# Performance work log

Hardware: AMD Instinct MI355X
Metric: run time of the kernel (lower is better)

The kernel has to match this reference:

```python
import jax, jax.numpy as jnp
import numpy as np

EPS = 1e-5

def inorm(x):
    # InstanceNorm1d(0) on 2D input: per-row normalization over last dim, biased var, no affine
    m = jnp.mean(x, axis=1, keepdims=True)
    v = jnp.mean((x - m) ** 2, axis=1, keepdims=True)
    return (x - m) / jnp.sqrt(v + EPS)

def spmm(rows, cols, vals, x, n_rows):
    # COO sparse @ dense: gather source rows, scale by edge weight, scatter-add to dest rows
    return jax.ops.segment_sum(vals[:, None] * x[cols], rows, num_segments=n_rows)

def setup_inputs() -> dict:
    key = jax.random.key(0)
    ks = jax.random.split(key, 16)
    NG, NI, D, E = 50000, 100000, 128, 800000
    B = 65536
    s = 0.1
    return {
        "group_ids": jax.random.randint(ks[0], (B,), 0, NG),
        "item_ids": jax.random.randint(ks[1], (B,), 0, NI),
        "gi_rows": jnp.sort(jax.random.randint(ks[2], (E,), 0, NG)),
        "gi_cols": jax.random.randint(ks[3], (E,), 0, NI),
        "gi_vals": jax.random.uniform(ks[4], (E,)),
        "gg_rows": jnp.sort(jax.random.randint(ks[5], (E,), 0, NG)),
        "gg_cols": jax.random.randint(ks[6], (E,), 0, NG),
        "gg_vals": jax.random.uniform(ks[7], (E,)),
        "g_feat": jax.random.normal(ks[8], (NG, D)),
        "i_feat": jax.random.normal(ks[9], (NI, D)),
        "emb_group": s * jax.random.normal(ks[10], (NG, D)),
        "emb_item": s * jax.random.normal(ks[11], (NI, D)),
        "W_w": s * jax.random.normal(ks[12], (D, D)),
        "W_b": jnp.zeros((D,)),
        "red_w": s * jax.random.normal(ks[13], (D, D)),
        "red_b": jnp.zeros((D,)),
        "item_fus_w": s * jax.random.normal(ks[14], (D, 2 * D)),
        "item_fus_b": jnp.zeros((D,)),
        "group_fus_w": s * jax.random.normal(ks[15], (D, 2 * D)),
        "group_fus_b": jnp.zeros((D,)),
    }

def reference(group_ids, item_ids, gi_rows, gi_cols, gi_vals, gg_rows, gg_cols, gg_vals,
              g_feat, i_feat, emb_group, emb_item, W_w, W_b, red_w, red_b,
              item_fus_w, item_fus_b, group_fus_w, group_fus_b):
    NG = g_feat.shape[0]
    L = 2
    sig = jax.nn.sigmoid

    def social_layer(x):
        # relu(W(spmm(gg, x)))
        agg = spmm(gg_rows, gg_cols, gg_vals, x, NG)
        return jax.nn.relu(agg @ W_w.T + W_b)

    # constructTrainGraph
    g2 = inorm(inorm(g_feat) @ red_w.T + red_b)
    i2 = inorm(inorm(i_feat) @ red_w.T + red_b)
    final_item = sig(jnp.concatenate([emb_item, i2], axis=1) @ item_fus_w.T + item_fus_b)
    g_from_items = sig(spmm(gi_rows, gi_cols, gi_vals, final_item, NG))
    fus_group = sig(jnp.concatenate([emb_group, g2], axis=1) @ group_fus_w.T + group_fus_b)
    first = sig(social_layer(fus_group))
    tmp = g_from_items + first
    second = sig(social_layer(first))
    tmp = tmp + second
    final_group = sig(tmp / L)

    # forward scoring
    all_neighbors = spmm(gg_rows, gg_cols, gg_vals, final_group, NG)
    ge = final_group[group_ids]
    ie = final_item[item_ids]
    ne = all_neighbors[group_ids]
    gamma = jnp.sum(ge * ie, axis=1)
    gamma_2 = jnp.sum(ne * ge, axis=1) + jnp.sum(ne * ie, axis=1)
    return gamma, gamma_2
```

## Files before the change

kernel.cpp:

```cpp
#include <hip/hip_runtime.h>
#include <hip/hip_bf16.h>

typedef __hip_bfloat16 bf16;
typedef __attribute__((ext_vector_type(8))) short bf16x8;
typedef __attribute__((ext_vector_type(4))) float f32x4;

#define D128 128

__device__ __forceinline__ float sigf(float x) {
    float e = __builtin_amdgcn_exp2f(-1.44269504f * x);
    return __builtin_amdgcn_rcpf(1.0f + e);
}

__device__ __forceinline__ short bf2s(bf16 h) { union { bf16 h; short s; } u; u.h = h; return u.s; }
__device__ __forceinline__ float s2f(short s) { union { short s; bf16 h; } u; u.s = s; return __bfloat162float(u.h); }

__device__ __forceinline__ float loadf(const void* p, size_t off, int isbf) {
    return isbf ? __bfloat162float(((const bf16*)p)[off]) : ((const float*)p)[off];
}

__global__ __launch_bounds__(256) void sniff_kernel(const unsigned short* __restrict__ g,
                                                    int* __restrict__ cnt) {
    int t = threadIdx.x;
    int c = 0;
    for (int i = t; i < 16384; i += 256) {
        unsigned short u = g[i];
        if ((u & 0x7F80u) == 0x7F80u) c++;
    }
    #pragma unroll
    for (int o = 32; o >= 1; o >>= 1) c += __shfl_xor(c, o);
    __shared__ int sh[4];
    if ((t & 63) == 0) sh[t >> 6] = c;
    __syncthreads();
    if (t == 0) *cnt = sh[0] + sh[1] + sh[2] + sh[3];
}

template <int KCH>
__global__ __launch_bounds__(256) void prep_w(const void* __restrict__ W,
                                              bf16x8* __restrict__ wf,
                                              const void* __restrict__ bias,
                                              float* __restrict__ bias_f,
                                              const int* __restrict__ cnt) {
    int isbf = (*cnt == 0);
    const int K = KCH * 32;
    int idx = blockIdx.x * 256 + threadIdx.x;
    const int total = 8 * KCH * 64;
    if (idx < total) {
        int t = idx / (KCH * 64);
        int c = (idx / 64) % KCH;
        int l = idx & 63;
        int row = t * 16 + (l & 15);
        int off = c * 32 + (l >> 4) * 8;
        bf16x8 r;
        if (isbf) {
            r = *reinterpret_cast<const bf16x8*>((const bf16*)W + (size_t)row * K + off);
        } else {
            const f32x4* f = reinterpret_cast<const f32x4*>((const float*)W + (size_t)row * K + off);
            f32x4 a = f[0], b = f[1];
            #pragma unroll
            for (int j = 0; j < 4; ++j) {
                r[j] = bf2s(__float2bfloat16(a[j]));
                r[4 + j] = bf2s(__float2bfloat16(b[j]));
            }
        }
        wf[idx] = r;
    }
    if (idx < D128) bias_f[idx] = loadf(bias, idx, isbf);
}

__global__ __launch_bounds__(256) void ngn_kernel(const void* __restrict__ X,
                                                  const bf16x8* __restrict__ wf,
                                                  const float* __restrict__ bias_f,
                                                  bf16* __restrict__ out, int N,
                                                  const int* __restrict__ cnt) {
    int isbf = (*cnt == 0);
    int tid = threadIdx.x;
    int wave = tid >> 6, lane = tid & 63;
    int quad = lane >> 4, l16 = lane & 15;
    int tile = blockIdx.x * 4 + wave;
    if (tile * 16 >= N) return;
    int mrow = tile * 16 + l16;

    float x[4][8];
    if (isbf) {
        #pragma unroll
        for (int c = 0; c < 4; ++c) {
            bf16x8 v = *reinterpret_cast<const bf16x8*>(
                (const bf16*)X + (size_t)mrow * D128 + c * 32 + quad * 8);
            #pragma unroll
            for (int j = 0; j < 8; ++j) x[c][j] = s2f(v[j]);
        }
    } else {
        #pragma unroll
        for (int c = 0; c < 4; ++c) {
            const f32x4* f = reinterpret_cast<const f32x4*>(
                (const float*)X + (size_t)mrow * D128 + c * 32 + quad * 8);
            f32x4 a = f[0], b = f[1];
            #pragma unroll
            for (int j = 0; j < 4; ++j) { x[c][j] = a[j]; x[c][4 + j] = b[j]; }
        }
    }
    float s = 0.f, ss = 0.f;
    #pragma unroll
    for (int c = 0; c < 4; ++c)
        #pragma unroll
        for (int j = 0; j < 8; ++j) { s += x[c][j]; ss += x[c][j] * x[c][j]; }
    s += __shfl_xor(s, 16); ss += __shfl_xor(ss, 16);
    s += __shfl_xor(s, 32); ss += __shfl_xor(ss, 32);
    float mean = s * (1.0f / 128.0f);
    float var = ss * (1.0f / 128.0f) - mean * mean;
    float rinv = rsqrtf(fmaxf(var, 0.f) + 1e-5f);

    bf16x8 af[4];
    #pragma unroll
    for (int c = 0; c < 4; ++c)
        #pragma unroll
        for (int j = 0; j < 8; ++j)
            af[c][j] = bf2s(__float2bfloat16((x[c][j] - mean) * rinv));

    f32x4 acc[8] = {};
    #pragma unroll
    for (int t = 0; t < 8; ++t)
        #pragma unroll
        for (int c = 0; c < 4; ++c)
            acc[t] = __builtin_amdgcn_mfma_f32_16x16x32_bf16(
                af[c], wf[(t * 4 + c) * 64 + lane], acc[t], 0, 0, 0);

    float vals[8][4];
    float ps[4] = {0, 0, 0, 0}, pss[4] = {0, 0, 0, 0};
    #pragma unroll
    for (int t = 0; t < 8; ++t) {
        float b = bias_f[t * 16 + l16];
        #pragma unroll
        for (int i = 0; i < 4; ++i) {
            float v = acc[t][i] + b;
            vals[t][i] = v;
            ps[i] += v; pss[i] += v * v;
        }
    }
    #pragma unroll
    for (int i = 0; i < 4; ++i) {
        #pragma unroll
        for (int o = 1; o < 16; o <<= 1) {
            ps[i] += __shfl_xor(ps[i], o);
            pss[i] += __shfl_xor(pss[i], o);
        }
    }
    #pragma unroll
    for (int i = 0; i < 4; ++i) {
        int row = tile * 16 + quad * 4 + i;
        float m2 = ps[i] * (1.0f / 128.0f);
        float v2 = pss[i] * (1.0f / 128.0f) - m2 * m2;
        float r2 = rsqrtf(fmaxf(v2, 0.f) + 1e-5f);
        #pragma unroll
        for (int t = 0; t < 8; ++t)
            out[(size_t)row * D128 + t * 16 + l16] =
                __float2bfloat16((vals[t][i] - m2) * r2);
    }
}

template <int KCH, int ACT, int A0T>
__global__ __launch_bounds__(256) void gemm_kernel(const void* __restrict__ A0,
                                                   const bf16* __restrict__ A1,
                                                   const bf16x8* __restrict__ wf,
                                                   const float* __restrict__ bias_f,
                                                   bf16* __restrict__ out, int N,
                                                   const int* __restrict__ cnt) {
    int isbf = (*cnt == 0);
    int tid = threadIdx.x;
    int wave = tid >> 6, lane = tid & 63;
    int quad = lane >> 4, l16 = lane & 15;
    int tile = blockIdx.x * 4 + wave;
    if (tile * 16 >= N) return;
    int mrow = tile * 16 + l16;

    bool a0bf = (A0T == 2) || (A0T == 1 && isbf);
    const int na = (KCH == 8) ? 4 : KCH;
    bf16x8 af[KCH];
    if (KCH == 8) {
        #pragma unroll
        for (int c = 4; c < KCH; ++c)
            af[c] = *reinterpret_cast<const bf16x8*>(
                A1 + (size_t)mrow * D128 + (c - 4) * 32 + quad * 8);
    }
    if (a0bf) {
        #pragma unroll
        for (int c = 0; c < na; ++c)
            af[c] = *reinterpret_cast<const bf16x8*>(
                (const bf16*)A0 + (size_t)mrow * D128 + c * 32 + quad * 8);
    } else {
        #pragma unroll
        for (int c = 0; c < na; ++c) {
            const f32x4* f = reinterpret_cast<const f32x4*>(
                (const float*)A0 + (size_t)mrow * D128 + c * 32 + quad * 8);
            f32x4 a = f[0], b = f[1];
            #pragma unroll
            for (int j = 0; j < 4; ++j) {
                af[c][j] = bf2s(__float2bfloat16(a[j]));
                af[c][4 + j] = bf2s(__float2bfloat16(b[j]));
            }
        }
    }

    f32x4 acc[8] = {};
    #pragma unroll
    for (int t = 0; t < 8; ++t)
        #pragma unroll
        for (int c = 0; c < KCH; ++c)
            acc[t] = __builtin_amdgcn_mfma_f32_16x16x32_bf16(
                af[c], wf[(t * KCH + c) * 64 + lane], acc[t], 0, 0, 0);

    #pragma unroll
    for (int t = 0; t < 8; ++t) {
        float b = bias_f[t * 16 + l16];
        #pragma unroll
        for (int i = 0; i < 4; ++i) {
            int row = tile * 16 + quad * 4 + i;
            float v = acc[t][i] + b;
            if (ACT == 1) v = sigf(v);
            else if (ACT == 2) v = sigf(fmaxf(v, 0.0f));
            out[(size_t)row * D128 + t * 16 + l16] = __float2bfloat16(v);
        }
    }
}

__global__ __launch_bounds__(256) void rowptr_kernel(const int* __restrict__ rows,
                                                     int* __restrict__ ptr,
                                                     int NR, int E) {
    int r = blockIdx.x * 256 + threadIdx.x;
    if (r > NR) return;
    int lo = 0, hi = E;
    while (lo < hi) {
        int mid = (lo + hi) >> 1;
        if (rows[mid] < r) lo = mid + 1; else hi = mid;
    }
    ptr[r] = lo;
}

#define SPMM_U 16
#define SPMM_RPW 4

template <int FM>
__device__ __forceinline__ void st_row(void* __restrict__ out, int r,
                                       int lane, float a0, float a1,
                                       const bf16* __restrict__ f1,
                                       const bf16* __restrict__ f2) {
    if (FM == 0) {
        float2 v; v.x = a0; v.y = a1;
        ((float2*)((float*)out + (size_t)r * D128))[lane] = v;
    } else if (FM == 1) {
        __hip_bfloat162 h;
        h.x = __float2bfloat16(a0);
        h.y = __float2bfloat16(a1);
        ((__hip_bfloat162*)((bf16*)out + (size_t)r * D128))[lane] = h;
    } else {
        __hip_bfloat162 h1 = ((const __hip_bfloat162*)(f1 + (size_t)r * D128))[lane];
        __hip_bfloat162 h2 = ((const __hip_bfloat162*)(f2 + (size_t)r * D128))[lane];
        float v0 = (sigf(a0) + __bfloat162float(h1.x) + __bfloat162float(h2.x)) * 0.5f;
        float v1 = (sigf(a1) + __bfloat162float(h1.y) + __bfloat162float(h2.y)) * 0.5f;
        __hip_bfloat162 h;
        h.x = __float2bfloat16(sigf(v0));
        h.y = __float2bfloat16(sigf(v1));
        ((__hip_bfloat162*)((bf16*)out + (size_t)r * D128))[lane] = h;
    }
}

template <int FM>
__device__ __forceinline__ void spmm_core(const int* __restrict__ rows,
                                          const int* __restrict__ ptr,
                                          const int* __restrict__ cols,
                                          const void* __restrict__ vals,
                                          const bf16* __restrict__ X,
                                          void* __restrict__ out,
                                          int r0, int r1, int lane, int isbf,
                                          const bf16* __restrict__ f1,
                                          const bf16* __restrict__ f2) {
    int e0 = __builtin_amdgcn_readfirstlane(ptr[r0]);
    int e1 = __builtin_amdgcn_readfirstlane(ptr[r1]);

    if (e0 == e1) {
        for (int z = r0; z < r1; ++z) st_row<FM>(out, z, lane, 0.f, 0.f, f1, f2);
        return;
    }

    int prev = __builtin_amdgcn_readfirstlane(rows[e0]);
    for (int z = r0; z < prev; ++z) st_row<FM>(out, z, lane, 0.f, 0.f, f1, f2);

    int u16 = lane & 15, grp = lane >> 4;
    int emax = e1 - 1;

    auto meta_ld = [&](int base) -> unsigned int {
        int e = base + u16;
        if (e > emax) e = emax;
        unsigned int v = 0;
        if (grp == 0) v = (unsigned int)cols[e];
        else if (grp == 1) v = (unsigned int)rows[e];
        else if (grp == 2)
            v = isbf ? (((unsigned int)((const unsigned short*)vals)[e]) << 16)
                     : ((const unsigned int*)vals)[e];
        return v;
    };

    unsigned int mv = meta_ld(e0);
    float a0 = 0.f, a1 = 0.f;
    for (int base = e0; base < e1; base += SPMM_U) {
        int nb = e1 - base;
        unsigned int xr[SPMM_U];
        #pragma unroll
        for (int u = 0; u < SPMM_U; ++u) {
            int cc = __builtin_amdgcn_readlane(mv, u);
            xr[u] = *((const unsigned int*)(X + (size_t)(unsigned)cc * D128) + lane);
        }
        int rr[SPMM_U];
        float vv[SPMM_U];
        #pragma unroll
        for (int u = 0; u < SPMM_U; ++u) {
            rr[u] = __builtin_amdgcn_readlane(mv, 16 + u);
            unsigned int vb = __builtin_amdgcn_readlane(mv, 32 + u);
            vv[u] = (u < nb) ? __uint_as_float(vb) : 0.f;
        }
        int nbase = base + SPMM_U;
        if (nbase < e1) mv = meta_ld(nbase);
        #pragma unroll
        for (int u = 0; u < SPMM_U; ++u) {
            if (rr[u] != prev) {
                st_row<FM>(out, prev, lane, a0, a1, f1, f2);
                for (int z = prev + 1; z < rr[u]; ++z)
                    st_row<FM>(out, z, lane, 0.f, 0.f, f1, f2);
                a0 = 0.f; a1 = 0.f;
                prev = rr[u];
            }
            __hip_bfloat162 x2 = *reinterpret_cast<const __hip_bfloat162*>(&xr[u]);
            a0 += vv[u] * __bfloat162float(x2.x);
            a1 += vv[u] * __bfloat162float(x2.y);
        }
    }
    st_row<FM>(out, prev, lane, a0, a1, f1, f2);
    for (int z = prev + 1; z < r1; ++z) st_row<FM>(out, z, lane, 0.f, 0.f, f1, f2);
}

template <int OUTBF>
__global__ __launch_bounds__(256) void spmm_hyb_kernel(const int* __restrict__ rows,
                                                       const int* __restrict__ ptr,
                                                       const int* __restrict__ cols,
                                                       const void* __restrict__ vals,
                                                       const bf16* __restrict__ X,
                                                       void* __restrict__ out, int NR,
                                                       const int* __restrict__ cnt) {
    int isbf = (*cnt == 0);
    int w = blockIdx.x * 4 + (threadIdx.x >> 6);
    int r0 = w * SPMM_RPW;
    if (r0 >= NR) return;
    int r1 = min(r0 + SPMM_RPW, NR);
    int lane = threadIdx.x & 63;
    spmm_core<OUTBF ? 1 : 0>(rows, ptr, cols, vals, X, out, r0, r1, lane, isbf,
                             nullptr, nullptr);
}

__global__ __launch_bounds__(256) void spmm_fg_kernel(const int* __restrict__ rows,
                                                      const int* __restrict__ ptr,
                                                      const int* __restrict__ cols,
                                                      const void* __restrict__ vals,
                                                      const bf16* __restrict__ X,
                                                      const bf16* __restrict__ f1,
                                                      const bf16* __restrict__ f2,
                                                      bf16* __restrict__ out, int NR,
                                                      const int* __restrict__ cnt) {
    int isbf = (*cnt == 0);
    int w = blockIdx.x * 4 + (threadIdx.x >> 6);
    int r0 = w * SPMM_RPW;
    if (r0 >= NR) return;
    int r1 = min(r0 + SPMM_RPW, NR);
    int lane = threadIdx.x & 63;
    spmm_core<3>(rows, ptr, cols, vals, X, out, r0, r1, lane, isbf, f1, f2);
}

__global__ __launch_bounds__(256) void score_kernel(const int* __restrict__ gids,
                                                    const int* __restrict__ iids,
                                                    const bf16* __restrict__ FG,
                                                    const bf16* __restrict__ FI,
                                                    const float* __restrict__ NB,
                                                    void* __restrict__ out, int Bn,
                                                    const int* __restrict__ cnt) {
    int isbf = (*cnt == 0);
    int w = blockIdx.x * 4 + (threadIdx.x >> 6);
    int lane = threadIdx.x & 63;
    if (w >= Bn) return;
    int g = gids[w];
    int it = iids[w];
    __hip_bfloat162 ge2 = ((const __hip_bfloat162*)(FG + (size_t)g * D128))[lane];
    __hip_bfloat162 ie2 = ((const __hip_bfloat162*)(FI + (size_t)it * D128))[lane];
    float2 ne2 = ((const float2*)(NB + (size_t)g * D128))[lane];
    float ge0 = __bfloat162float(ge2.x), ge1 = __bfloat162float(ge2.y);
    float ie0 = __bfloat162float(ie2.x), ie1 = __bfloat162float(ie2.y);
    float gi = ge0 * ie0 + ge1 * ie1;
    float ng = ne2.x * ge0 + ne2.y * ge1;
    float ni = ne2.x * ie0 + ne2.y * ie1;
    #pragma unroll
    for (int o = 32; o >= 1; o >>= 1) {
        gi += __shfl_xor(gi, o);
        ng += __shfl_xor(ng, o);
        ni += __shfl_xor(ni, o);
    }
    if (lane == 0) {
        if (isbf) {
            ((bf16*)out)[w] = __float2bfloat16(gi);
            ((bf16*)out)[Bn + w] = __float2bfloat16(ng + ni);
        } else {
            ((float*)out)[w] = gi;
            ((float*)out)[Bn + w] = ng + ni;
        }
    }
}

extern "C" void kernel_launch(void* const* d_in, const int* in_sizes, int n_in,
                              void* d_out, int out_size, void* d_ws, size_t ws_size,
                              hipStream_t stream) {
    const int* group_ids = (const int*)d_in[0];
    const int* item_ids  = (const int*)d_in[1];
    const int* gi_rows   = (const int*)d_in[2];
    const int* gi_cols   = (const int*)d_in[3];
    const void* gi_vals  = d_in[4];
    const int* gg_rows   = (const int*)d_in[5];
    const int* gg_cols   = (const int*)d_in[6];
    const void* gg_vals  = d_in[7];
    const void* g_feat   = d_in[8];
    const void* i_feat   = d_in[9];
    const void* emb_group = d_in[10];
    const void* emb_item  = d_in[11];
    const void* W_w       = d_in[12];
    const void* W_b       = d_in[13];
    const void* red_w     = d_in[14];
    const void* red_b     = d_in[15];
    const void* item_fus_w = d_in[16];
    const void* item_fus_b = d_in[17];
    const void* group_fus_w = d_in[18];
    const void* group_fus_b = d_in[19];

    const int Bn = in_sizes[0];
    const int E  = in_sizes[2];
    const int NG = in_sizes[8] / D128;
    const int NI = in_sizes[9] / D128;

    const size_t NGD2 = (size_t)NG * D128 * 2;
    const size_t NID2 = (size_t)NI * D128 * 2;
    const size_t NGD4 = (size_t)NG * D128 * 4;
    char* ws = (char*)d_ws;
    void* agg    = (void*)(ws);
    bf16* itemB  = (bf16*)(ws + NGD4);
    bf16* gB     = (bf16*)(ws + NGD4 + NID2);
    bf16* firstB = (bf16*)(ws + NGD4 + NID2 + NGD2);
    bf16* secondB= (bf16*)(ws + NGD4 + NID2 + 2 * NGD2);
    char* xtra   = ws + NGD4 + NID2 + 3 * NGD2;
    bf16x8* wf_red  = (bf16x8*)(xtra);
    bf16x8* wf_W    = (bf16x8*)(xtra + 32 * 1024);
    bf16x8* wf_ifus = (bf16x8*)(xtra + 64 * 1024);
    bf16x8* wf_gfus = (bf16x8*)(xtra + 128 * 1024);
    float* b_red  = (float*)(xtra + 192 * 1024);
    float* b_W    = (float*)(xtra + 192 * 1024 + 512);
    float* b_ifus = (float*)(xtra + 192 * 1024 + 1024);
    float* b_gfus = (float*)(xtra + 192 * 1024 + 1536);
    int*  cnt     = (int*)(xtra + 194 * 1024);
    int*  ptrGG   = (int*)(xtra + 196 * 1024);
    int*  ptrGI   = ptrGG + (NG + 1);

    const int tilesG = NG >> 4, tilesI = NI >> 4;
    const int gridG = (tilesG + 3) / 4;
    const int gridI = (tilesI + 3) / 4;
    const int gridPtr = (NG + 1 + 255) / 256;
    const int nwSp = (NG + SPMM_RPW - 1) / SPMM_RPW;
    const int gridSp = (nwSp + 3) / 4;

    sniff_kernel<<<1, 256, 0, stream>>>((const unsigned short*)g_feat, cnt);
    rowptr_kernel<<<gridPtr, 256, 0, stream>>>(gg_rows, ptrGG, NG, E);
    rowptr_kernel<<<gridPtr, 256, 0, stream>>>(gi_rows, ptrGI, NG, E);
    prep_w<4><<<8, 256, 0, stream>>>(red_w, wf_red, red_b, b_red, cnt);
    prep_w<4><<<8, 256, 0, stream>>>(W_w, wf_W, W_b, b_W, cnt);
    prep_w<8><<<16, 256, 0, stream>>>(item_fus_w, wf_ifus, item_fus_b, b_ifus, cnt);
    prep_w<8><<<16, 256, 0, stream>>>(group_fus_w, wf_gfus, group_fus_b, b_gfus, cnt);
    ngn_kernel<<<gridG, 256, 0, stream>>>(g_feat, wf_red, b_red, gB, NG, cnt);
    ngn_kernel<<<gridI, 256, 0, stream>>>(i_feat, wf_red, b_red, itemB, NI, cnt);
    gemm_kernel<8, 1, 1><<<gridI, 256, 0, stream>>>(emb_item, itemB, wf_ifus,
                                                    b_ifus, itemB, NI, cnt);
    gemm_kernel<8, 1, 1><<<gridG, 256, 0, stream>>>(emb_group, gB, wf_gfus,
                                                    b_gfus, gB, NG, cnt);
    spmm_hyb_kernel<1><<<gridSp, 256, 0, stream>>>(gg_rows, ptrGG, gg_cols, gg_vals,
                                                   gB, agg, NG, cnt);
    gemm_kernel<4, 2, 2><<<gridG, 256, 0, stream>>>(agg, nullptr, wf_W, b_W,
                                                    firstB, NG, cnt);
    spmm_hyb_kernel<1><<<gridSp, 256, 0, stream>>>(gg_rows, ptrGG, gg_cols, gg_vals,
                                                   firstB, agg, NG, cnt);
    gemm_kernel<4, 2, 2><<<gridG, 256, 0, stream>>>(agg, nullptr, wf_W, b_W,
                                                    secondB, NG, cnt);
    spmm_fg_kernel<<<gridSp, 256, 0, stream>>>(gi_rows, ptrGI, gi_cols, gi_vals,
                                               itemB, firstB, secondB, gB, NG, cnt);
    spmm_hyb_kernel<0><<<gridSp, 256, 0, stream>>>(gg_rows, ptrGG, gg_cols, gg_vals,
                                                   gB, agg, NG, cnt);
    score_kernel<<<(Bn + 3) / 4, 256, 0, stream>>>(group_ids, item_ids, gB, itemB,
                                                   (const float*)agg, d_out, Bn, cnt);
}
```

Before: 470.1 us.

## Stage GEMM weight fragments through double-buffered LDS shared by all waves

The GEMM kernel now loads the weight fragments cooperatively into a double-buffered shared-memory tile, one output column tile at a time, instead of every wave reading them from global memory. The next tile's weights are prefetched into registers while the current tile's MFMAs run. Inactive tail waves stay alive so they can take part in the barriers. This cuts redundant global/L2 weight traffic per block, at the cost of eight block-wide barriers and extra LDS traffic in a kernel that is mostly memory-bound on activations.

```diff
diff --git a/kernel.cpp b/kernel.cpp
--- a/kernel.cpp
+++ b/kernel.cpp
@@ -166,13 +166,14 @@
                                                    const float* __restrict__ bias_f,
                                                    bf16* __restrict__ out, int N,
                                                    const int* __restrict__ cnt) {
+    __shared__ bf16x8 wlds[2][KCH * 64];
     int isbf = (*cnt == 0);
     int tid = threadIdx.x;
     int wave = tid >> 6, lane = tid & 63;
     int quad = lane >> 4, l16 = lane & 15;
     int tile = blockIdx.x * 4 + wave;
-    if (tile * 16 >= N) return;
-    int mrow = tile * 16 + l16;
+    bool active = (tile * 16 < N);
+    int mrow = active ? tile * 16 + l16 : l16;
 
     bool a0bf = (A0T == 2) || (A0T == 1 && isbf);
     const int na = (KCH == 8) ? 4 : KCH;
@@ -202,24 +203,50 @@
         }
     }
 
+    const int SL = KCH / 4;
+    bf16x8 streg[SL];
+    #pragma unroll
+    for (int k = 0; k < SL; ++k) streg[k] = wf[k * 256 + tid];
+    #pragma unroll
+    for (int k = 0; k < SL; ++k) wlds[0][k * 256 + tid] = streg[k];
+    __syncthreads();
+
     f32x4 acc[8] = {};
     #pragma unroll
-    for (int t = 0; t < 8; ++t)
+    for (int t = 0; t < 8; ++t) {
+        if (t + 1 < 8) {
+            #pragma unroll
+            for (int k = 0; k < SL; ++k)
+                streg[k] = wf[(t + 1) * (KCH * 64) + k * 256 + tid];
+        }
+        bf16x8 wfr[KCH];
+        #pragma unroll
+        for (int c = 0; c < KCH; ++c)
+            wfr[c] = wlds[t & 1][c * 64 + lane];
         #pragma unroll
         for (int c = 0; c < KCH; ++c)
             acc[t] = __builtin_amdgcn_mfma_f32_16x16x32_bf16(
-                af[c], wf[(t * KCH + c) * 64 + lane], acc[t], 0, 0, 0);
-
-    #pragma unroll
-    for (int t = 0; t < 8; ++t) {
-        float b = bias_f[t * 16 + l16];
-        #pragma unroll
-        for (int i = 0; i < 4; ++i) {
-            int row = tile * 16 + quad * 4 + i;
-            float v = acc[t][i] + b;
-            if (ACT == 1) v = sigf(v);
-            else if (ACT == 2) v = sigf(fmaxf(v, 0.0f));
-            out[(size_t)row * D128 + t * 16 + l16] = __float2bfloat16(v);
+                af[c], wfr[c], acc[t], 0, 0, 0);
+        if (t + 1 < 8) {
+            #pragma unroll
+            for (int k = 0; k < SL; ++k)
+                wlds[(t + 1) & 1][k * 256 + tid] = streg[k];
+        }
+        __syncthreads();
+    }
+
+    if (active) {
+        #pragma unroll
+        for (int t = 0; t < 8; ++t) {
+            float b = bias_f[t * 16 + l16];
+            #pragma unroll
+            for (int i = 0; i < 4; ++i) {
+                int row = tile * 16 + quad * 4 + i;
+                float v = acc[t][i] + b;
+                if (ACT == 1) v = sigf(v);
+                else if (ACT == 2) v = sigf(fmaxf(v, 0.0f));
+                out[(size_t)row * D128 + t * 16 + l16] = __float2bfloat16(v);
+            }
         }
     }
 }
```

Measured after the change: 456.5 us. -2.9%, faster.
